# Kernel tuning notes

Measured on AMD Instinct MI355X. Metric: run time of the kernel, lower is better.

The kernel has to match this reference:

```python
import jax, jax.numpy as jnp
import numpy as np

N_NODES = 100000


def gcn_conv(x, src, dst, ew, W, b, n):
    """PyG GCNConv: self-loops (weight 1), symmetric norm, linear + bias.
    src/dst/ew already include self-loops."""
    xw = x @ W  # [N, out]
    deg = jax.ops.segment_sum(ew, dst, num_segments=n)  # in-degree with weights
    dinv = jnp.where(deg > 0, jax.lax.rsqrt(deg), 0.0)
    norm = dinv[src] * ew * dinv[dst]  # [E]
    msgs = xw[src] * norm[:, None]  # gather + scale
    out = jax.ops.segment_sum(msgs, dst, num_segments=n)  # scatter-add
    return out + b


def setup_inputs() -> dict:
    key = jax.random.key(0)
    k1, k2, k3, k4, k5 = jax.random.split(key, 5)
    x = jax.random.normal(k1, (N_NODES, 512), dtype=jnp.float32)
    edge_index = jax.random.randint(k2, (2, 3200000), 0, N_NODES, dtype=jnp.int64)
    edge_weight = jax.random.uniform(k3, (3200000,), dtype=jnp.float32)
    W1 = jax.random.normal(k4, (512, 64), dtype=jnp.float32) * (1.0 / np.sqrt(512))
    b1 = jnp.zeros((64,), dtype=jnp.float32)
    W2 = jax.random.normal(k5, (64, 20), dtype=jnp.float32) * (1.0 / np.sqrt(64))
    b2 = jnp.zeros((20,), dtype=jnp.float32)
    return {"x": x, "edge_index": edge_index, "edge_weight": edge_weight,
            "W1": W1, "b1": b1, "W2": W2, "b2": b2}


def reference(x, edge_index, edge_weight, W1, b1, W2, b2):
    n = x.shape[0]
    loops = jnp.arange(n, dtype=edge_index.dtype)
    src = jnp.concatenate([edge_index[0], loops])
    dst = jnp.concatenate([edge_index[1], loops])
    ew = jnp.concatenate([edge_weight, jnp.ones((n,), dtype=edge_weight.dtype)])
    h = gcn_conv(x, src, dst, ew, W1, b1, n)
    h = jax.nn.relu(h)  # dropout is identity in eval mode
    h = gcn_conv(h, src, dst, ew, W2, b2, n)
    return jax.nn.softmax(h, axis=-1)
```

## Files before the change

### kernel.cpp

```cpp
#include <hip/hip_runtime.h>
#include <hip/hip_fp16.h>
#include <math.h>

#define FIN 512
#define H   64
#define C   20

typedef _Float16 half8 __attribute__((ext_vector_type(8)));
typedef float floatx4 __attribute__((ext_vector_type(4)));

__device__ __forceinline__ int detect_m64(const int* __restrict__ ei) {
    int nz = 0;
    #pragma unroll
    for (int i = 0; i < 32; i++) nz |= ei[2 * i + 1];
    return nz == 0;
}

__device__ __forceinline__ int edge_val(const int* __restrict__ ei, long long idx, int m64) {
    return m64 ? ei[2 * idx] : ei[(int)idx];
}

__global__ void init_kernel(const float* __restrict__ W, _Float16* __restrict__ W1T,
                            unsigned long long* __restrict__ packed, int N) {
    int tid = blockIdx.x * 256 + threadIdx.x;
    if (tid < H * FIN) {
        int n = tid >> 9, k = tid & 511;
        W1T[tid] = (_Float16)W[k * H + n];
    }
    if (tid < N) packed[tid] = 0ULL;
}

#define FIXSCALE 268435456.0f
#define KC 64
#define GM 64
#define HE 2048
__global__ __launch_bounds__(256, 8) void fused_gemm1_hist_kernel(
        const float* __restrict__ x, const _Float16* __restrict__ W1T,
        __half* __restrict__ xwh, int N,
        const int* __restrict__ ei, const float* __restrict__ ew,
        unsigned long long* __restrict__ packed, int* __restrict__ rank,
        int E, int GB, int HB) {
    __shared__ _Float16 xsh[GM][72];
    __shared__ _Float16 wsh[64][72];

    int nb = blockIdx.x;
    int minB = (GB < HB) ? GB : HB;
    int isHist, roleId;
    if (nb < 2 * minB) { isHist = !(nb & 1); roleId = nb >> 1; }
    else { int r = nb - 2 * minB; isHist = (HB > GB); roleId = minB + r; }

    if (isHist) {
        int m64 = detect_m64(ei);
        long long base = (long long)roleId * HE + threadIdx.x;
        int d[8]; float w[8];
        #pragma unroll
        for (int u = 0; u < 8; u++) {
            long long e = base + u * 256;
            if (e < E) { d[u] = edge_val(ei, (long long)E + e, m64); w[u] = ew[e]; }
            else d[u] = -1;
        }
        unsigned long long old[8];
        #pragma unroll
        for (int u = 0; u < 8; u++)
            if (d[u] >= 0) {
                unsigned long long add = (1ULL << 40) |
                    (unsigned long long)(w[u] * FIXSCALE + 0.5f);
                old[u] = atomicAdd(&packed[d[u]], add);
            }
        #pragma unroll
        for (int u = 0; u < 8; u++)
            if (d[u] >= 0) rank[base + u * 256] = (int)(old[u] >> 40);
        return;
    }

    int tid  = threadIdx.x;
    int wave = tid >> 6;
    int lane = tid & 63;
    int quad = lane >> 4;
    int l16  = lane & 15;
    int row0 = roleId * GM;

    floatx4 acc[4];
    #pragma unroll
    for (int ct = 0; ct < 4; ct++) acc[ct] = (floatx4){0.f, 0.f, 0.f, 0.f};

    int col4  = (tid & 15) * 4;
    int rbase = tid >> 4;
    int wn = tid >> 2;
    int wk = (tid & 3) * 16;

    for (int k0 = 0; k0 < FIN; k0 += KC) {
        #pragma unroll
        for (int it = 0; it < 4; it++) {
            int row = rbase + it * 16;
            int grow = row0 + row; if (grow >= N) grow = N - 1;
            float4 v = *(const float4*)&x[(long long)grow * FIN + k0 + col4];
            _Float16* p = &xsh[row][col4];
            p[0] = (_Float16)v.x; p[1] = (_Float16)v.y;
            p[2] = (_Float16)v.z; p[3] = (_Float16)v.w;
        }
        *(half8*)&wsh[wn][wk]     = *(const half8*)&W1T[wn * FIN + k0 + wk];
        *(half8*)&wsh[wn][wk + 8] = *(const half8*)&W1T[wn * FIN + k0 + wk + 8];
        __syncthreads();
        #pragma unroll
        for (int kk = 0; kk < KC; kk += 32) {
            half8 a0 = *(const half8*)&xsh[wave * 16 + l16][kk + quad * 8];
            #pragma unroll
            for (int ct = 0; ct < 4; ct++) {
                half8 b = *(const half8*)&wsh[ct * 16 + l16][kk + quad * 8];
                acc[ct] = __builtin_amdgcn_mfma_f32_16x16x32_f16(a0, b, acc[ct], 0, 0, 0);
            }
        }
        __syncthreads();
    }
    #pragma unroll
    for (int ct = 0; ct < 4; ct++)
        #pragma unroll
        for (int r = 0; r < 4; r++) {
            int grow = row0 + wave * 16 + quad * 4 + r;
            if (grow < N)
                xwh[(long long)grow * H + ct * 16 + l16] = __float2half(acc[ct][r]);
        }
}

__global__ void block_sums_kernel(const unsigned long long* __restrict__ packed,
                                  int* __restrict__ bsum, int N) {
    __shared__ int lds[256];
    int t = threadIdx.x;
    int base = blockIdx.x * 1024 + t * 4;
    int s = 0;
    #pragma unroll
    for (int k = 0; k < 4; k++) { int i = base + k; if (i < N) s += (int)(packed[i] >> 40); }
    lds[t] = s; __syncthreads();
    for (int off = 128; off > 0; off >>= 1) {
        if (t < off) lds[t] += lds[t + off];
        __syncthreads();
    }
    if (t == 0) bsum[blockIdx.x] = lds[0];
}

__global__ void scan_local_kernel(const unsigned long long* __restrict__ packed,
                                  const int* __restrict__ bsum,
                                  int* __restrict__ rowptr, float* __restrict__ dinv,
                                  int N, int E) {
    __shared__ int lds[256];
    int t = threadIdx.x, bid = blockIdx.x;
    lds[t] = (t < bid) ? bsum[t] : 0;
    __syncthreads();
    for (int off = 128; off > 0; off >>= 1) {
        if (t < off) lds[t] += lds[t + off];
        __syncthreads();
    }
    int bpre = lds[0];
    __syncthreads();

    int base = bid * 1024 + t * 4;
    int c[4]; int s = 0;
    #pragma unroll
    for (int k = 0; k < 4; k++) {
        int i = base + k;
        if (i < N) {
            unsigned long long v = packed[i];
            c[k] = (int)(v >> 40);
            dinv[i] = rsqrtf((float)(v & ((1ULL << 40) - 1)) * (1.0f / FIXSCALE) + 1.0f);
        } else c[k] = 0;
        s += c[k];
    }
    lds[t] = s; __syncthreads();
    for (int off = 1; off < 256; off <<= 1) {
        int add = (t >= off) ? lds[t - off] : 0;
        __syncthreads();
        lds[t] += add;
        __syncthreads();
    }
    int start = bpre + lds[t] - s;
    #pragma unroll
    for (int k = 0; k < 4; k++) {
        int i = base + k;
        if (i < N) { rowptr[i] = start; start += c[k]; }
    }
    if (bid == 0 && t == 0) rowptr[N] = E;
}

__global__ void fill2_kernel(const int* __restrict__ ei, const float* __restrict__ ew,
                             const float* __restrict__ dinv, const int* __restrict__ rowptr,
                             const int* __restrict__ rank, int2* __restrict__ edata, int E) {
    int m64 = detect_m64(ei);
    long long t = (long long)blockIdx.x * blockDim.x + threadIdx.x;
    long long e0 = 2 * t;
    if (e0 >= E) return;
    int s0, s1, d0, d1;
    if (m64) {
        int4 sp = *(const int4*)&ei[2 * e0];
        int4 dp = *(const int4*)&ei[2 * (long long)E + 2 * e0];
        s0 = sp.x; s1 = sp.z; d0 = dp.x; d1 = dp.z;
    } else {
        int2 sp = *(const int2*)&ei[e0];
        int2 dp = *(const int2*)&ei[(long long)E + e0];
        s0 = sp.x; s1 = sp.y; d0 = dp.x; d1 = dp.y;
    }
    float2 w = *(const float2*)&ew[e0];
    int2  rk = *(const int2*)&rank[e0];
    edata[rowptr[d0] + rk.x] = make_int2(s0, __float_as_int(dinv[s0] * w.x * dinv[d0]));
    if (e0 + 1 < E)
        edata[rowptr[d1] + rk.y] = make_int2(s1, __float_as_int(dinv[s1] * w.y * dinv[d1]));
}

#define A1_NODES 8
__global__ __launch_bounds__(256) void agg1g2_kernel(
        const int* __restrict__ rowptr, const int2* __restrict__ edata,
        const __half* __restrict__ xwh, const float* __restrict__ dinv,
        const float* __restrict__ b1, const float* __restrict__ W2,
        __half* __restrict__ xw2h, int N) {
    __shared__ float hs[A1_NODES][H + 2];
    __shared__ float w2s[H * C];
    for (int t = threadIdx.x; t < H * C; t += 256) w2s[t] = W2[t];
    int hw = threadIdx.x >> 5;
    int l  = threadIdx.x & 31;
    int i  = blockIdx.x * A1_NODES + hw;
    if (i < N) {
        int start = rowptr[i], end = rowptr[i + 1];
        float a0 = 0.f, a1 = 0.f;
        int j = start;
        for (; j + 3 < end; j += 4) {
            int2 e0 = edata[j], e1 = edata[j + 1], e2 = edata[j + 2], e3 = edata[j + 3];
            float2 v0 = __half22float2(*(const __half2*)&xwh[(long long)e0.x * H + 2 * l]);
            float2 v1 = __half22float2(*(const __half2*)&xwh[(long long)e1.x * H + 2 * l]);
            float2 v2 = __half22float2(*(const __half2*)&xwh[(long long)e2.x * H + 2 * l]);
            float2 v3 = __half22float2(*(const __half2*)&xwh[(long long)e3.x * H + 2 * l]);
            float n0 = __int_as_float(e0.y), n1 = __int_as_float(e1.y);
            float n2 = __int_as_float(e2.y), n3 = __int_as_float(e3.y);
            a0 = fmaf(v0.x, n0, a0); a1 = fmaf(v0.y, n0, a1);
            a0 = fmaf(v1.x, n1, a0); a1 = fmaf(v1.y, n1, a1);
            a0 = fmaf(v2.x, n2, a0); a1 = fmaf(v2.y, n2, a1);
            a0 = fmaf(v3.x, n3, a0); a1 = fmaf(v3.y, n3, a1);
        }
        for (; j < end; j++) {
            int2 e0 = edata[j];
            float2 v0 = __half22float2(*(const __half2*)&xwh[(long long)e0.x * H + 2 * l]);
            float n0 = __int_as_float(e0.y);
            a0 = fmaf(v0.x, n0, a0); a1 = fmaf(v0.y, n0, a1);
        }
        float di = dinv[i]; float sl = di * di;
        float2 vs = __half22float2(*(const __half2*)&xwh[(long long)i * H + 2 * l]);
        a0 = fmaf(vs.x, sl, a0); a1 = fmaf(vs.y, sl, a1);
        float2 bb = *(const float2*)&b1[2 * l];
        hs[hw][2 * l]     = fmaxf(a0 + bb.x, 0.f);
        hs[hw][2 * l + 1] = fmaxf(a1 + bb.y, 0.f);
    }
    __syncthreads();
    int t = threadIdx.x;
    if (t < A1_NODES * C) {
        int r = t / C, c = t % C;
        int node = blockIdx.x * A1_NODES + r;
        if (node < N) {
            float acc = 0.f;
            #pragma unroll
            for (int k = 0; k < H; k++) acc = fmaf(hs[r][k], w2s[k * C + c], acc);
            xw2h[(long long)node * C + c] = __float2half(acc);
        }
    }
}

__global__ void agg2_final_kernel(const int* __restrict__ rowptr, const int2* __restrict__ edata,
                                  const __half* __restrict__ xw2h, const float* __restrict__ dinv,
                                  const float* __restrict__ b2, float* __restrict__ out, int N) {
    long long gid = (long long)blockIdx.x * blockDim.x + threadIdx.x;
    int wid = (int)(gid >> 6);
    int half = (threadIdx.x & 63) >> 5;
    int l = threadIdx.x & 31;
    int i = wid * 2 + half;
    float acc = 0.f;
    bool active = (i < N) && (l < C);
    if (active) {
        int start = rowptr[i], end = rowptr[i + 1];
        int j = start;
        for (; j + 3 < end; j += 4) {
            int2 e0 = edata[j], e1 = edata[j + 1], e2 = edata[j + 2], e3 = edata[j + 3];
            float v0 = __half2float(xw2h[(long long)e0.x * C + l]);
            float v1 = __half2float(xw2h[(long long)e1.x * C + l]);
            float v2 = __half2float(xw2h[(long long)e2.x * C + l]);
            float v3 = __half2float(xw2h[(long long)e3.x * C + l]);
            acc = fmaf(v0, __int_as_float(e0.y), acc);
            acc = fmaf(v1, __int_as_float(e1.y), acc);
            acc = fmaf(v2, __int_as_float(e2.y), acc);
            acc = fmaf(v3, __int_as_float(e3.y), acc);
        }
        for (; j < end; j++) {
            int2 e = edata[j];
            acc = fmaf(__half2float(xw2h[(long long)e.x * C + l]), __int_as_float(e.y), acc);
        }
        float di = dinv[i];
        acc = fmaf(__half2float(xw2h[(long long)i * C + l]), di * di, acc);
        acc += b2[l];
    }
    float v = active ? acc : -1e30f;
    float mx = v;
    #pragma unroll
    for (int off = 16; off >= 1; off >>= 1) mx = fmaxf(mx, __shfl_xor(mx, off, 32));
    float ex = active ? expf(v - mx) : 0.f;
    float sm = ex;
    #pragma unroll
    for (int off = 16; off >= 1; off >>= 1) sm += __shfl_xor(sm, off, 32);
    if (active) out[(long long)i * C + l] = ex / sm;
}

static inline size_t align256(size_t x) { return (x + 255) & ~(size_t)255; }

extern "C" void kernel_launch(void* const* d_in, const int* in_sizes, int n_in,
                              void* d_out, int out_size, void* d_ws, size_t ws_size,
                              hipStream_t stream) {
    const float* x  = (const float*)d_in[0];
    const int*   ei = (const int*)d_in[1];
    const float* ew = (const float*)d_in[2];
    const float* W1 = (const float*)d_in[3];
    const float* b1 = (const float*)d_in[4];
    const float* W2 = (const float*)d_in[5];
    const float* b2 = (const float*)d_in[6];
    float* out = (float*)d_out;

    int N = in_sizes[0] / FIN;
    int E = in_sizes[2];
    int NB = (N + 1023) / 1024;

    char* ws = (char*)d_ws;
    size_t off = 0;
    unsigned long long* packed = (unsigned long long*)(ws + off); off = align256(off + (size_t)N * 8);
    float*    dinv   = (float*)(ws + off);    off = align256(off + (size_t)N * 4);
    int*      bsum   = (int*)(ws + off);      off = align256(off + (size_t)NB * 4);
    int*      rowptr = (int*)(ws + off);      off = align256(off + (size_t)(N + 1) * 4);
    int2*     edata  = (int2*)(ws + off);     off = align256(off + (size_t)E * 8);
    _Float16* W1T    = (_Float16*)(ws + off); off = align256(off + (size_t)H * FIN * 2);
    __half*   xw1h   = (__half*)(ws + off);   off = align256(off + (size_t)N * H * 2);
    int*      rank   = (int*)(ws + off);      off = align256(off + (size_t)E * 4);
    __half*   xw2h   = (__half*)(ws + off);   off = align256(off + (size_t)N * C * 2);

    int initBlocks = (max(H * FIN, N) + 255) / 256;
    init_kernel<<<initBlocks, 256, 0, stream>>>(W1, W1T, packed, N);

    int GB = (N + GM - 1) / GM;
    int HB = (E + HE - 1) / HE;
    fused_gemm1_hist_kernel<<<GB + HB, 256, 0, stream>>>(
        x, W1T, xw1h, N, ei, ew, packed, rank, E, GB, HB);

    block_sums_kernel<<<NB, 256, 0, stream>>>(packed, bsum, N);
    scan_local_kernel<<<NB, 256, 0, stream>>>(packed, bsum, rowptr, dinv, N, E);

    fill2_kernel<<<(int)(((long long)(E + 1) / 2 + 255) / 256), 256, 0, stream>>>(
        ei, ew, dinv, rowptr, rank, edata, E);

    agg1g2_kernel<<<(N + A1_NODES - 1) / A1_NODES, 256, 0, stream>>>(
        rowptr, edata, xw1h, dinv, b1, W2, xw2h, N);

    int waves2 = (N + 1) / 2;
    agg2_final_kernel<<<(int)(((long long)waves2 * 64 + 255) / 256), 256, 0, stream>>>(
        rowptr, edata, xw2h, dinv, b2, out, N);
}
```

Measured before the change: 652.3 us.

## Pack dst into rank, move dinv normalization out of CSR fill, pad layer-2 features

The histogram pass now packs the destination node index together with the edge's rank, so the fill kernel no longer reloads dst from edge_index or gathers dinv. Edge data keeps only the raw weight. The symmetric normalization is refactored: layer 1 applies dinv[src] per edge at gather time plus dinv[dst] once per node. Layer 2 pre-scales features by dinv[src] and stores them in a 32-wide padded fp16 buffer, so agg2 only multiplies by dinv[dst] once. This trades random dinv gathers in fill2 for extra dinv gathers in agg1, and the 17-bit dst packing assumes N fits in 131072.

```diff
diff --git a/kernel.cpp b/kernel.cpp
--- a/kernel.cpp
+++ b/kernel.cpp
@@ -5,6 +5,7 @@
 #define FIN 512
 #define H   64
 #define C   20
+#define CP  32
 
 typedef _Float16 half8 __attribute__((ext_vector_type(8)));
 typedef float floatx4 __attribute__((ext_vector_type(4)));
@@ -38,7 +39,7 @@
         const float* __restrict__ x, const _Float16* __restrict__ W1T,
         __half* __restrict__ xwh, int N,
         const int* __restrict__ ei, const float* __restrict__ ew,
-        unsigned long long* __restrict__ packed, int* __restrict__ rank,
+        unsigned long long* __restrict__ packed, int* __restrict__ rankdst,
         int E, int GB, int HB) {
     __shared__ _Float16 xsh[GM][72];
     __shared__ _Float16 wsh[64][72];
@@ -69,7 +70,8 @@
             }
         #pragma unroll
         for (int u = 0; u < 8; u++)
-            if (d[u] >= 0) rank[base + u * 256] = (int)(old[u] >> 40);
+            if (d[u] >= 0)
+                rankdst[base + u * 256] = ((int)(old[u] >> 40) << 17) | d[u];
         return;
     }
 
@@ -183,27 +185,27 @@
 }
 
 __global__ void fill2_kernel(const int* __restrict__ ei, const float* __restrict__ ew,
-                             const float* __restrict__ dinv, const int* __restrict__ rowptr,
-                             const int* __restrict__ rank, int2* __restrict__ edata, int E) {
+                             const int* __restrict__ rowptr,
+                             const int* __restrict__ rankdst, int2* __restrict__ edata, int E) {
     int m64 = detect_m64(ei);
     long long t = (long long)blockIdx.x * blockDim.x + threadIdx.x;
     long long e0 = 2 * t;
     if (e0 >= E) return;
-    int s0, s1, d0, d1;
+    int s0, s1;
     if (m64) {
         int4 sp = *(const int4*)&ei[2 * e0];
-        int4 dp = *(const int4*)&ei[2 * (long long)E + 2 * e0];
-        s0 = sp.x; s1 = sp.z; d0 = dp.x; d1 = dp.z;
+        s0 = sp.x; s1 = sp.z;
     } else {
         int2 sp = *(const int2*)&ei[e0];
-        int2 dp = *(const int2*)&ei[(long long)E + e0];
-        s0 = sp.x; s1 = sp.y; d0 = dp.x; d1 = dp.y;
+        s0 = sp.x; s1 = sp.y;
     }
     float2 w = *(const float2*)&ew[e0];
-    int2  rk = *(const int2*)&rank[e0];
-    edata[rowptr[d0] + rk.x] = make_int2(s0, __float_as_int(dinv[s0] * w.x * dinv[d0]));
+    int2  rd = *(const int2*)&rankdst[e0];
+    int d0 = rd.x & 131071, rk0 = rd.x >> 17;
+    int d1 = rd.y & 131071, rk1 = rd.y >> 17;
+    edata[rowptr[d0] + rk0] = make_int2(s0, __float_as_int(w.x));
     if (e0 + 1 < E)
-        edata[rowptr[d1] + rk.y] = make_int2(s1, __float_as_int(dinv[s1] * w.y * dinv[d1]));
+        edata[rowptr[d1] + rk1] = make_int2(s1, __float_as_int(w.y));
 }
 
 #define A1_NODES 8
@@ -211,7 +213,7 @@
         const int* __restrict__ rowptr, const int2* __restrict__ edata,
         const __half* __restrict__ xwh, const float* __restrict__ dinv,
         const float* __restrict__ b1, const float* __restrict__ W2,
-        __half* __restrict__ xw2h, int N) {
+        __half* __restrict__ zp, int N) {
     __shared__ float hs[A1_NODES][H + 2];
     __shared__ float w2s[H * C];
     for (int t = threadIdx.x; t < H * C; t += 256) w2s[t] = W2[t];
@@ -224,12 +226,13 @@
         int j = start;
         for (; j + 3 < end; j += 4) {
             int2 e0 = edata[j], e1 = edata[j + 1], e2 = edata[j + 2], e3 = edata[j + 3];
+            float ds0 = dinv[e0.x], ds1 = dinv[e1.x], ds2 = dinv[e2.x], ds3 = dinv[e3.x];
             float2 v0 = __half22float2(*(const __half2*)&xwh[(long long)e0.x * H + 2 * l]);
             float2 v1 = __half22float2(*(const __half2*)&xwh[(long long)e1.x * H + 2 * l]);
             float2 v2 = __half22float2(*(const __half2*)&xwh[(long long)e2.x * H + 2 * l]);
             float2 v3 = __half22float2(*(const __half2*)&xwh[(long long)e3.x * H + 2 * l]);
-            float n0 = __int_as_float(e0.y), n1 = __int_as_float(e1.y);
-            float n2 = __int_as_float(e2.y), n3 = __int_as_float(e3.y);
+            float n0 = __int_as_float(e0.y) * ds0, n1 = __int_as_float(e1.y) * ds1;
+            float n2 = __int_as_float(e2.y) * ds2, n3 = __int_as_float(e3.y) * ds3;
             a0 = fmaf(v0.x, n0, a0); a1 = fmaf(v0.y, n0, a1);
             a0 = fmaf(v1.x, n1, a0); a1 = fmaf(v1.y, n1, a1);
             a0 = fmaf(v2.x, n2, a0); a1 = fmaf(v2.y, n2, a1);
@@ -238,32 +241,33 @@
         for (; j < end; j++) {
             int2 e0 = edata[j];
             float2 v0 = __half22float2(*(const __half2*)&xwh[(long long)e0.x * H + 2 * l]);
-            float n0 = __int_as_float(e0.y);
+            float n0 = __int_as_float(e0.y) * dinv[e0.x];
             a0 = fmaf(v0.x, n0, a0); a1 = fmaf(v0.y, n0, a1);
         }
-        float di = dinv[i]; float sl = di * di;
+        float di = dinv[i];
         float2 vs = __half22float2(*(const __half2*)&xwh[(long long)i * H + 2 * l]);
-        a0 = fmaf(vs.x, sl, a0); a1 = fmaf(vs.y, sl, a1);
+        a0 = fmaf(vs.x, di, a0); a1 = fmaf(vs.y, di, a1);
         float2 bb = *(const float2*)&b1[2 * l];
-        hs[hw][2 * l]     = fmaxf(a0 + bb.x, 0.f);
-        hs[hw][2 * l + 1] = fmaxf(a1 + bb.y, 0.f);
+        hs[hw][2 * l]     = fmaxf(fmaf(a0, di, bb.x), 0.f);
+        hs[hw][2 * l + 1] = fmaxf(fmaf(a1, di, bb.y), 0.f);
     }
     __syncthreads();
-    int t = threadIdx.x;
-    if (t < A1_NODES * C) {
-        int r = t / C, c = t % C;
-        int node = blockIdx.x * A1_NODES + r;
-        if (node < N) {
+    int r = threadIdx.x >> 5, c = threadIdx.x & 31;
+    int node = blockIdx.x * A1_NODES + r;
+    if (node < N) {
+        float v = 0.f;
+        if (c < C) {
             float acc = 0.f;
             #pragma unroll
             for (int k = 0; k < H; k++) acc = fmaf(hs[r][k], w2s[k * C + c], acc);
-            xw2h[(long long)node * C + c] = __float2half(acc);
-        }
+            v = acc * dinv[node];
+        }
+        zp[(long long)node * CP + c] = __float2half(v);
     }
 }
 
 __global__ void agg2_final_kernel(const int* __restrict__ rowptr, const int2* __restrict__ edata,
-                                  const __half* __restrict__ xw2h, const float* __restrict__ dinv,
+                                  const __half* __restrict__ zp, const float* __restrict__ dinv,
                                   const float* __restrict__ b2, float* __restrict__ out, int N) {
     long long gid = (long long)blockIdx.x * blockDim.x + threadIdx.x;
     int wid = (int)(gid >> 6);
@@ -277,10 +281,10 @@
         int j = start;
         for (; j + 3 < end; j += 4) {
             int2 e0 = edata[j], e1 = edata[j + 1], e2 = edata[j + 2], e3 = edata[j + 3];
-            float v0 = __half2float(xw2h[(long long)e0.x * C + l]);
-            float v1 = __half2float(xw2h[(long long)e1.x * C + l]);
-            float v2 = __half2float(xw2h[(long long)e2.x * C + l]);
-            float v3 = __half2float(xw2h[(long long)e3.x * C + l]);
+            float v0 = __half2float(zp[(long long)e0.x * CP + l]);
+            float v1 = __half2float(zp[(long long)e1.x * CP + l]);
+            float v2 = __half2float(zp[(long long)e2.x * CP + l]);
+            float v3 = __half2float(zp[(long long)e3.x * CP + l]);
             acc = fmaf(v0, __int_as_float(e0.y), acc);
             acc = fmaf(v1, __int_as_float(e1.y), acc);
             acc = fmaf(v2, __int_as_float(e2.y), acc);
@@ -288,11 +292,10 @@
         }
         for (; j < end; j++) {
             int2 e = edata[j];
-            acc = fmaf(__half2float(xw2h[(long long)e.x * C + l]), __int_as_float(e.y), acc);
-        }
-        float di = dinv[i];
-        acc = fmaf(__half2float(xw2h[(long long)i * C + l]), di * di, acc);
-        acc += b2[l];
+            acc = fmaf(__half2float(zp[(long long)e.x * CP + l]), __int_as_float(e.y), acc);
+        }
+        acc += __half2float(zp[(long long)i * CP + l]);
+        acc = fmaf(acc, dinv[i], b2[l]);
     }
     float v = active ? acc : -1e30f;
     float mx = v;
@@ -326,14 +329,14 @@
     char* ws = (char*)d_ws;
     size_t off = 0;
     unsigned long long* packed = (unsigned long long*)(ws + off); off = align256(off + (size_t)N * 8);
-    float*    dinv   = (float*)(ws + off);    off = align256(off + (size_t)N * 4);
-    int*      bsum   = (int*)(ws + off);      off = align256(off + (size_t)NB * 4);
-    int*      rowptr = (int*)(ws + off);      off = align256(off + (size_t)(N + 1) * 4);
-    int2*     edata  = (int2*)(ws + off);     off = align256(off + (size_t)E * 8);
-    _Float16* W1T    = (_Float16*)(ws + off); off = align256(off + (size_t)H * FIN * 2);
-    __half*   xw1h   = (__half*)(ws + off);   off = align256(off + (size_t)N * H * 2);
-    int*      rank   = (int*)(ws + off);      off = align256(off + (size_t)E * 4);
-    __half*   xw2h   = (__half*)(ws + off);   off = align256(off + (size_t)N * C * 2);
+    float*    dinv    = (float*)(ws + off);    off = align256(off + (size_t)N * 4);
+    int*      bsum    = (int*)(ws + off);      off = align256(off + (size_t)NB * 4);
+    int*      rowptr  = (int*)(ws + off);      off = align256(off + (size_t)(N + 1) * 4);
+    int2*     edata   = (int2*)(ws + off);     off = align256(off + (size_t)E * 8);
+    _Float16* W1T     = (_Float16*)(ws + off); off = align256(off + (size_t)H * FIN * 2);
+    __half*   xw1h    = (__half*)(ws + off);   off = align256(off + (size_t)N * H * 2);
+    int*      rankdst = (int*)(ws + off);      off = align256(off + (size_t)E * 4);
+    __half*   zp      = (__half*)(ws + off);   off = align256(off + (size_t)N * CP * 2);
 
     int initBlocks = (max(H * FIN, N) + 255) / 256;
     init_kernel<<<initBlocks, 256, 0, stream>>>(W1, W1T, packed, N);
@@ -341,18 +344,18 @@
     int GB = (N + GM - 1) / GM;
     int HB = (E + HE - 1) / HE;
     fused_gemm1_hist_kernel<<<GB + HB, 256, 0, stream>>>(
-        x, W1T, xw1h, N, ei, ew, packed, rank, E, GB, HB);
+        x, W1T, xw1h, N, ei, ew, packed, rankdst, E, GB, HB);
 
     block_sums_kernel<<<NB, 256, 0, stream>>>(packed, bsum, N);
     scan_local_kernel<<<NB, 256, 0, stream>>>(packed, bsum, rowptr, dinv, N, E);
 
     fill2_kernel<<<(int)(((long long)(E + 1) / 2 + 255) / 256), 256, 0, stream>>>(
-        ei, ew, dinv, rowptr, rank, edata, E);
+        ei, ew, rowptr, rankdst, edata, E);
 
     agg1g2_kernel<<<(N + A1_NODES - 1) / A1_NODES, 256, 0, stream>>>(
-        rowptr, edata, xw1h, dinv, b1, W2, xw2h, N);
+        rowptr, edata, xw1h, dinv, b1, W2, zp, N);
 
     int waves2 = (N + 1) / 2;
     agg2_final_kernel<<<(int)(((long long)waves2 * 64 + 255) / 256), 256, 0, stream>>>(
-        rowptr, edata, xw2h, dinv, b2, out, N);
-}
+        rowptr, edata, zp, dinv, b2, out, N);
+}
```

Result: faster. 636.4 us (-2.4%).
